# Optimization experiments

Measured on AMD Instinct MI355X. Metric: run time of the kernel, lower is better.

## Reference

```python
import jax, jax.numpy as jnp
import numpy as np
import math

B, L, D, H, DFF = 2, 2048, 1024, 16, 4096

def _mha(xq, xkv, Wq, bq, Wk, bk, Wv, bv, Wo, bo, mask, h):
    # xq: [B,Lq,D], xkv: [B,Lk,D], mask: [B,1,Lq,Lk] bool
    b, lq, d = xq.shape
    dk = d // h
    q = (xq @ Wq + bq).reshape(b, lq, h, dk).transpose(0, 2, 1, 3)        # [B,h,Lq,dk]
    k = (xkv @ Wk + bk).reshape(b, -1, h, dk).transpose(0, 2, 1, 3)       # [B,h,Lk,dk]
    v = (xkv @ Wv + bv).reshape(b, -1, h, dk).transpose(0, 2, 1, 3)       # [B,h,Lk,dk]
    scores = jnp.einsum('bhqd,bhkd->bhqk', q, k) / jnp.sqrt(jnp.float32(dk))
    scores = jnp.where(mask, scores, jnp.float32(-1e9))                   # masked_fill(mask==0, -1e9)
    prob = jax.nn.softmax(scores, axis=-1)
    out = jnp.einsum('bhqk,bhkd->bhqd', prob, v)
    out = out.transpose(0, 2, 1, 3).reshape(b, lq, d)
    return out @ Wo + bo

def setup_inputs() -> dict:
    key = jax.random.key(0)
    ks = jax.random.split(key, 16)
    s = 0.02
    inp = {
        'tgt': jax.random.normal(ks[0], (B, L, D), jnp.float32),
        'encoder_out': jax.random.normal(ks[1], (B, L, D), jnp.float32),
        'tgt_mask': jnp.broadcast_to(jnp.tril(jnp.ones((L, L), bool)), (B, 1, L, L)),
        'src_tgt_mask': jnp.ones((B, 1, L, L), bool),
    }
    names = ['sWq','sWk','sWv','sWo','cWq','cWk','cWv','cWo']
    for i, n in enumerate(names):
        inp[n] = s * jax.random.normal(ks[2 + i], (D, D), jnp.float32)
        inp['sb' + n[2] if n[0] == 's' else 'cb' + n[2]] = jnp.zeros((D,), jnp.float32)
    inp['W1'] = s * jax.random.normal(ks[10], (D, DFF), jnp.float32)
    inp['b1'] = jnp.zeros((DFF,), jnp.float32)
    inp['W2'] = s * jax.random.normal(ks[11], (DFF, D), jnp.float32)
    inp['b2'] = jnp.zeros((D,), jnp.float32)
    return inp

def reference(tgt, encoder_out, tgt_mask, src_tgt_mask,
              sWq, sbq, sWk, sbk, sWv, sbv, sWo, sbo,
              cWq, cbq, cWk, cbk, cWv, cbv, cWo, cbo,
              W1, b1, W2, b2):
    # residual 1: masked self-attention (no norm)
    x = tgt + _mha(tgt, tgt, sWq, sbq, sWk, sbk, sWv, sbv, sWo, sbo, tgt_mask, H)
    # residual 2: cross-attention over encoder_out
    x = x + _mha(x, encoder_out, cWq, cbq, cWk, cbk, cWv, cbv, cWo, cbo, src_tgt_mask, H)
    # residual 3: position-wise FFN with ReLU
    x = x + (jax.nn.relu(x @ W1 + b1) @ W2 + b2)
    return x
```

## Files before the change

kernel.cpp:

```cpp
#include <hip/hip_runtime.h>

typedef unsigned short u16;
typedef unsigned int u32;
typedef __attribute__((ext_vector_type(8))) short short8;
typedef __attribute__((ext_vector_type(8))) __bf16 bf16x8;
typedef __attribute__((ext_vector_type(4))) float f32x4;
typedef __attribute__((ext_vector_type(4))) u16 u16x4;
typedef __attribute__((ext_vector_type(2))) u32 u32x2;

#define GLD16(gp, lp) __builtin_amdgcn_global_load_lds( \
    (const __attribute__((address_space(1))) unsigned int*)(gp), \
    (__attribute__((address_space(3))) unsigned int*)(lp), 16, 0, 0)

#if defined(__has_builtin) && __has_builtin(__builtin_amdgcn_exp2f)
#define EXP2(x) __builtin_amdgcn_exp2f(x)
#else
static __device__ __forceinline__ float exp2_asm(float x){
  float r; asm("v_exp_f32 %0, %1" : "=v"(r) : "v"(x)); return r;
}
#define EXP2(x) exp2_asm(x)
#endif

__device__ __forceinline__ float bf2f(u16 u){
  unsigned x = ((unsigned)u) << 16; float f; __builtin_memcpy(&f, &x, 4); return f;
}
__device__ __forceinline__ u16 f2bf(float f){
  unsigned x; __builtin_memcpy(&x, &f, 4);
  x += 0x7fffu + ((x >> 16) & 1u);
  return (u16)(x >> 16);
}
__device__ __forceinline__ u32 pkhi(float lo, float hi){
  u32 a, b; __builtin_memcpy(&a, &lo, 4); __builtin_memcpy(&b, &hi, 4);
  return __builtin_amdgcn_perm(b, a, 0x07060302u);
}
__device__ __forceinline__ f32x4 mfma_bf16(short8 a, short8 b, f32x4 c){
  return __builtin_amdgcn_mfma_f32_16x16x32_bf16(
      __builtin_bit_cast(bf16x8, a), __builtin_bit_cast(bf16x8, b), c, 0, 0, 0);
}

__global__ __launch_bounds__(256) void k_conv(const float* __restrict__ s, u16* __restrict__ d, int n){
  int i4 = (blockIdx.x * 256 + threadIdx.x) * 4;
  if (i4 < n){
    float4 v = *(const float4*)(s + i4);
    u16x4 o; o.x = f2bf(v.x); o.y = f2bf(v.y); o.z = f2bf(v.z); o.w = f2bf(v.w);
    *(u16x4*)(d + i4) = o;
  }
}

__global__ __launch_bounds__(256) void k_transpose(const float* __restrict__ s, u16* __restrict__ d, int K, int N){
  __shared__ float t[32][33];
  int bx = blockIdx.x * 32, by = blockIdx.y * 32;
  int x = threadIdx.x & 31, y = threadIdx.x >> 5;
  #pragma unroll
  for (int i = 0; i < 4; i++)
    t[y + i*8][x] = s[(size_t)(by + y + i*8) * N + bx + x];
  __syncthreads();
  #pragma unroll
  for (int i = 0; i < 4; i++)
    d[(size_t)(bx + y + i*8) * K + by + x] = f2bf(t[x][y + i*8]);
}

struct TP8 { const float* s[8]; u16* d[8]; };
__global__ __launch_bounds__(256) void k_transpose8(TP8 p){
  __shared__ float t[32][33];
  const float* s = p.s[blockIdx.z];
  u16* d = p.d[blockIdx.z];
  int bx = blockIdx.x * 32, by = blockIdx.y * 32;
  int x = threadIdx.x & 31, y = threadIdx.x >> 5;
  #pragma unroll
  for (int i = 0; i < 4; i++)
    t[y + i*8][x] = s[(size_t)(by + y + i*8) * 1024 + bx + x];
  __syncthreads();
  #pragma unroll
  for (int i = 0; i < 4; i++)
    d[(size_t)(bx + y + i*8) * 1024 + by + x] = f2bf(t[x][y + i*8]);
}

__global__ __launch_bounds__(256) void k_packbias(
    const float* __restrict__ sbq, const float* __restrict__ sbk,
    const float* __restrict__ sbv, const float* __restrict__ cbk,
    const float* __restrict__ cbv, float* __restrict__ pbS,
    float* __restrict__ pbC){
  int i = blockIdx.x * 256 + threadIdx.x;
  if (i < 3072) pbS[i] = (i < 1024) ? sbq[i] : (i < 2048 ? sbk[i-1024] : sbv[i-2048]);
  if (i < 2048) pbC[i] = (i < 1024) ? cbk[i] : cbv[i-1024];
}

template<int EPI, int BM, int BN, int KU>
__global__ __launch_bounds__(256, 2) void k_gemm_bt(
    const u16* __restrict__ A, const u16* __restrict__ BT,
    const float* __restrict__ bias, const float* __restrict__ resid,
    float* __restrict__ outF, u16* __restrict__ outB,
    int M, int N, int K, int vt_start, u16* __restrict__ Vt){
  constexpr int MI = BM / 32, NI = BN / 32;
  __shared__ u16 As[2*KU][BM*32];
  __shared__ u16 Bs[2*KU][BN*32];
  int tid = threadIdx.x, wave = tid >> 6, lane = tid & 63;
  int bm = blockIdx.x * BM, bn = blockIdx.y * BN;
  int wm = (wave & 1) * (BM/2), wn = (wave >> 1) * (BN/2);
  int l15 = lane & 15, quad = lane >> 4;

  f32x4 z = {0.f, 0.f, 0.f, 0.f};
  f32x4 acc[MI][NI];
  #pragma unroll
  for (int a = 0; a < MI; a++)
    #pragma unroll
    for (int b = 0; b < NI; b++) acc[a][b] = z;

  int sr = wave*16 + (lane >> 2);
  int sc = ((lane & 3) ^ ((lane >> 3) & 3)) * 8;
  const u16* Ag = A  + (size_t)(bm + sr) * K + sc;
  const u16* Bg = BT + (size_t)(bn + sr) * K + sc;
  int NKP = (K >> 5) / KU;
  int xsw = (l15 >> 1) & 3;

  #pragma unroll
  for (int u = 0; u < KU; u++){
    #pragma unroll
    for (int i = 0; i < BM/64; i++)
      GLD16(Ag + (size_t)(i*64)*K + u*32, &As[u][(wave*16 + i*64) * 32]);
    #pragma unroll
    for (int i = 0; i < BN/64; i++)
      GLD16(Bg + (size_t)(i*64)*K + u*32, &Bs[u][(wave*16 + i*64) * 32]);
  }

  for (int kt = 0; kt < NKP; kt++){
    __syncthreads();
    int cur = (kt & 1) * KU;
    if (kt + 1 < NKP){
      int nb = cur ^ KU;
      #pragma unroll
      for (int u = 0; u < KU; u++){
        int k0 = ((kt + 1) * KU + u) * 32;
        #pragma unroll
        for (int i = 0; i < BM/64; i++)
          GLD16(Ag + (size_t)(i*64)*K + k0, &As[nb+u][(wave*16 + i*64) * 32]);
        #pragma unroll
        for (int i = 0; i < BN/64; i++)
          GLD16(Bg + (size_t)(i*64)*K + k0, &Bs[nb+u][(wave*16 + i*64) * 32]);
      }
    }
    #pragma unroll
    for (int u = 0; u < KU; u++){
      short8 af[MI], bf[NI];
      #pragma unroll
      for (int mi = 0; mi < MI; mi++)
        af[mi] = *(const short8*)&As[cur+u][(wm + mi*16 + l15)*32 + (quad ^ xsw)*8];
      #pragma unroll
      for (int ni = 0; ni < NI; ni++)
        bf[ni] = *(const short8*)&Bs[cur+u][(wn + ni*16 + l15)*32 + (quad ^ xsw)*8];
      #pragma unroll
      for (int mi = 0; mi < MI; mi++)
        #pragma unroll
        for (int ni = 0; ni < NI; ni++)
          acc[mi][ni] = mfma_bf16(af[mi], bf[ni], acc[mi][ni]);
    }
  }

  #pragma unroll
  for (int mi = 0; mi < MI; mi++){
    #pragma unroll
    for (int ni = 0; ni < NI; ni++){
      int col = bn + wn + ni*16 + l15;
      float bv = bias[col];
      if (EPI == 0 && col >= vt_start){
        int vc = col - vt_start;
        int hh = vc >> 6, dd = vc & 63;
        int row0 = bm + wm + mi*16 + quad*4;
        int bb = row0 >> 11, ll = row0 & 2047;
        u16x4 vv;
        #pragma unroll
        for (int r = 0; r < 4; r++) vv[r] = f2bf(acc[mi][ni][r] + bv);
        *(u16x4*)&Vt[(((size_t)bb*16 + hh)*64 + dd)*2048 + ll] = vv;
      } else {
        #pragma unroll
        for (int r = 0; r < 4; r++){
          int row = bm + wm + mi*16 + quad*4 + r;
          float v = acc[mi][ni][r] + bv;
          if (EPI == 1) v = v > 0.f ? v : 0.f;
          size_t idx = (size_t)row * N + col;
          if (EPI >= 2) v += resid[idx];
          if (EPI == 2 || EPI == 3) outF[idx] = v;
          if (EPI != 3) outB[idx] = f2bf(v);
        }
      }
    }
  }
}

template<bool CAUSAL>
__global__ __launch_bounds__(256, 2) void k_flash(
    const u16* __restrict__ Q, int ldq,
    const u16* __restrict__ Kg, int ldk,
    const u16* __restrict__ Vt,
    u16* __restrict__ O, int ldo){
  __shared__ u16 Ks[2][128*64];
  __shared__ u16 Vs[2][64*128];
  __shared__ u16 Ps[128*64];
  int tid = threadIdx.x, wave = tid >> 6, lane = tid & 63;
  int l15 = lane & 15, quad = lane >> 4;
  int bx = blockIdx.x;
  int qt = CAUSAL ? ((bx & 1) ? (15 - (bx >> 1)) : (bx >> 1)) : bx;
  int bh = blockIdx.y;
  int b = bh >> 4, h = bh & 15;
  size_t bL = (size_t)b * 2048;
  const u16* qp = Q  + (bL + qt*128) * (size_t)ldq + h*64;
  const u16* kp = Kg + bL * (size_t)ldk + h*64;
  const u16* vtp = Vt + (size_t)bh * 64 * 2048;
  int wm = wave * 32;

  const float QSCALE = 0.125f * 1.44269504088896f;
  short8 qf[2][2];
  #pragma unroll
  for (int mi = 0; mi < 2; mi++)
    #pragma unroll
    for (int ks = 0; ks < 2; ks++){
      short8 t = *(const short8*)(qp + (size_t)(wm + mi*16 + l15)*ldq + ks*32 + quad*8);
      #pragma unroll
      for (int j = 0; j < 8; j++)
        t[j] = (short)f2bf(bf2f((u16)t[j]) * QSCALE);
      qf[mi][ks] = t;
    }

  f32x4 z = {0.f, 0.f, 0.f, 0.f};
  f32x4 o[2][4];
  float mrow[2], lrow[2];
  #pragma unroll
  for (int mi = 0; mi < 2; mi++){ mrow[mi] = -3.0e38f; lrow[mi] = 0.f; }
  #pragma unroll
  for (int mi = 0; mi < 2; mi++)
    #pragma unroll
    for (int nd = 0; nd < 4; nd++) o[mi][nd] = z;

  int nkt = CAUSAL ? (qt + 1) : 16;
  int cg = ((lane & 7) ^ ((lane >> 3) & 7)) * 8;
  #pragma unroll
  for (int i = 0; i < 4; i++){
    int r = i*32 + wave*8 + (lane >> 3);
    GLD16(kp + (size_t)r * ldk + cg, &Ks[0][(i*32 + wave*8) * 64]);
  }
  #pragma unroll
  for (int i = 0; i < 4; i++){
    int d0 = i*16 + wave*4;
    int d = d0 + (lane >> 4);
    int j = lane & 15;
    int chunk = (j & 8) | ((j ^ (d & 7)) & 7);
    GLD16(vtp + (size_t)d*2048 + chunk*8, &Vs[0][d0*128]);
  }

  for (int kt = 0; kt < nkt; kt++){
    __syncthreads();
    int cur = kt & 1;
    if (kt + 1 < nkt){
      int nb = cur ^ 1;
      #pragma unroll
      for (int i = 0; i < 4; i++){
        int r = i*32 + wave*8 + (lane >> 3);
        GLD16(kp + (size_t)((kt+1)*128 + r) * ldk + cg, &Ks[nb][(i*32 + wave*8) * 64]);
      }
      #pragma unroll
      for (int i = 0; i < 4; i++){
        int d0 = i*16 + wave*4;
        int d = d0 + (lane >> 4);
        int j = lane & 15;
        int chunk = (j & 8) | ((j ^ (d & 7)) & 7);
        GLD16(vtp + (size_t)d*2048 + (kt+1)*128 + chunk*8, &Vs[nb][d0*128]);
      }
    }

    f32x4 s[2][8];
    #pragma unroll
    for (int mi = 0; mi < 2; mi++)
      #pragma unroll
      for (int nk = 0; nk < 8; nk++) s[mi][nk] = z;
    #pragma unroll
    for (int ks = 0; ks < 2; ks++){
      short8 kf[8];
      #pragma unroll
      for (int nk = 0; nk < 8; nk++){
        int row = nk*16 + l15;
        kf[nk] = *(const short8*)&Ks[cur][row*64 + (((ks*4 + quad) ^ (row & 7)))*8];
      }
      #pragma unroll
      for (int mi = 0; mi < 2; mi++)
        #pragma unroll
        for (int nk = 0; nk < 8; nk++)
          s[mi][nk] = mfma_bf16(kf[nk], qf[mi][ks], s[mi][nk]);
    }

    if (CAUSAL && kt == qt){
      #pragma unroll
      for (int mi = 0; mi < 2; mi++){
        int q = wm + mi*16 + l15;
        #pragma unroll
        for (int nk = 0; nk < 8; nk++)
          #pragma unroll
          for (int r = 0; r < 4; r++){
            int key = nk*16 + quad*4 + r;
            if (key > q) s[mi][nk][r] = -1e30f;
          }
      }
    }

    #pragma unroll
    for (int mi = 0; mi < 2; mi++){
      float mx = s[mi][0][0];
      #pragma unroll
      for (int nk = 0; nk < 8; nk++)
        #pragma unroll
        for (int r = 0; r < 4; r++) mx = fmaxf(mx, s[mi][nk][r]);
      mx = fmaxf(mx, __shfl_xor(mx, 16));
      mx = fmaxf(mx, __shfl_xor(mx, 32));
      if (!__all(mx - mrow[mi] <= 8.f)){
        float mnew = fmaxf(mrow[mi], mx);
        float alpha = EXP2(mrow[mi] - mnew);
        mrow[mi] = mnew;
        lrow[mi] *= alpha;
        #pragma unroll
        for (int r = 0; r < 4; r++){
          float ar = __shfl(alpha, quad*20 + r);
          #pragma unroll
          for (int nd = 0; nd < 4; nd++) o[mi][nd][r] *= ar;
        }
      }
      float ls = 0.f;
      #pragma unroll
      for (int nk = 0; nk < 8; nk++)
        #pragma unroll
        for (int r = 0; r < 4; r++){
          float p = EXP2(s[mi][nk][r] - mrow[mi]);
          s[mi][nk][r] = p;
          ls += p;
        }
      ls += __shfl_xor(ls, 16);
      ls += __shfl_xor(ls, 32);
      lrow[mi] += ls;
    }

    #pragma unroll
    for (int half = 0; half < 2; half++){
      #pragma unroll
      for (int mi = 0; mi < 2; mi++){
        int row = wm + mi*16 + l15;
        #pragma unroll
        for (int nkl = 0; nkl < 4; nkl++){
          int nk = half*4 + nkl;
          u32x2 pw;
          pw.x = pkhi(s[mi][nk][0], s[mi][nk][1]);
          pw.y = pkhi(s[mi][nk][2], s[mi][nk][3]);
          int c = nkl*4 + quad;
          int phys = c ^ (row & 14);
          *(u32x2*)&Ps[row*64 + phys*4] = pw;
        }
      }
      #pragma unroll
      for (int kcl = 0; kcl < 2; kcl++){
        int kc = half*2 + kcl;
        short8 vf[4], pf[2];
        #pragma unroll
        for (int nd = 0; nd < 4; nd++){
          int d = nd*16 + l15;
          int cc = kc*4 + quad;
          int phys = (cc & 8) | ((cc ^ (d & 7)) & 7);
          vf[nd] = *(const short8*)&Vs[cur][d*128 + phys*8];
        }
        #pragma unroll
        for (int mi = 0; mi < 2; mi++){
          int row = wm + mi*16 + l15;
          int pc = kcl*8 + quad*2;
          int pphys = pc ^ (row & 14);
          pf[mi] = *(const short8*)&Ps[row*64 + pphys*4];
        }
        #pragma unroll
        for (int mi = 0; mi < 2; mi++)
          #pragma unroll
          for (int nd = 0; nd < 4; nd++)
            o[mi][nd] = mfma_bf16(pf[mi], vf[nd], o[mi][nd]);
      }
    }
  }

  u16* op = O + (bL + qt*128) * (size_t)ldo + h*64;
  #pragma unroll
  for (int mi = 0; mi < 2; mi++){
    float invl = 1.f / lrow[mi];
    #pragma unroll
    for (int r = 0; r < 4; r++){
      float ir = __shfl(invl, quad*20 + r);
      #pragma unroll
      for (int nd = 0; nd < 4; nd++)
        op[(size_t)(wm + mi*16 + quad*4 + r)*ldo + nd*16 + l15] = f2bf(o[mi][nd][r] * ir);
    }
  }
}

extern "C" void kernel_launch(void* const* d_in, const int* in_sizes, int n_in,
                              void* d_out, int out_size, void* d_ws, size_t ws_size,
                              hipStream_t stream){
  (void)in_sizes; (void)n_in; (void)out_size; (void)ws_size;
  const float* tgt = (const float*)d_in[0];
  const float* enc = (const float*)d_in[1];
  const float* sWq = (const float*)d_in[4];  const float* sbq = (const float*)d_in[5];
  const float* sWk = (const float*)d_in[6];  const float* sbk = (const float*)d_in[7];
  const float* sWv = (const float*)d_in[8];  const float* sbv = (const float*)d_in[9];
  const float* sWo = (const float*)d_in[10]; const float* sbo = (const float*)d_in[11];
  const float* cWq = (const float*)d_in[12]; const float* cbq = (const float*)d_in[13];
  const float* cWk = (const float*)d_in[14]; const float* cbk = (const float*)d_in[15];
  const float* cWv = (const float*)d_in[16]; const float* cbv = (const float*)d_in[17];
  const float* cWo = (const float*)d_in[18]; const float* cbo = (const float*)d_in[19];
  const float* W1  = (const float*)d_in[20]; const float* b1  = (const float*)d_in[21];
  const float* W2  = (const float*)d_in[22]; const float* b2  = (const float*)d_in[23];
  float* out = (float*)d_out;

  const int M = 4096;
  const int NEVER = 1 << 30;
  char* w = (char*)d_ws;
  auto alloc = [&](size_t bytes)->void*{ void* p = w; w += (bytes + 255) & ~(size_t)255; return p; };
  u16* tb    = (u16*)alloc((size_t)M*1024*2);
  u16* eb    = (u16*)alloc((size_t)M*1024*2);
  u16* qkv   = (u16*)alloc((size_t)M*3072*2);
  u16* ao    = (u16*)alloc((size_t)M*1024*2);
  u16* xb    = (u16*)alloc((size_t)M*1024*2);
  float* x1f = (float*)alloc((size_t)M*1024*4);
  u16* hbuf  = (u16*)alloc((size_t)M*4096*2);
  u16* VtS   = (u16*)alloc((size_t)32*64*2048*2);
  u16* VtC   = (u16*)alloc((size_t)32*64*2048*2);
  u16* sQKVT = (u16*)alloc((size_t)3072*1024*2);
  u16* sWoT  = (u16*)alloc((size_t)1024*1024*2);
  u16* cWqT  = (u16*)alloc((size_t)1024*1024*2);
  u16* cKVT  = (u16*)alloc((size_t)2048*1024*2);
  u16* cWoT  = (u16*)alloc((size_t)1024*1024*2);
  u16* W1T   = (u16*)alloc((size_t)4096*1024*2);
  u16* W2T   = (u16*)alloc((size_t)1024*4096*2);
  float* pbS = (float*)alloc(3072*4);
  float* pbC = (float*)alloc(2048*4);
  u16* cq  = tb;
  u16* ckv = qkv;

  k_conv<<<dim3(4096), 256, 0, stream>>>(tgt, tb, M*1024);
  k_conv<<<dim3(4096), 256, 0, stream>>>(enc, eb, M*1024);
  TP8 tp;
  tp.s[0]=sWq; tp.s[1]=sWk; tp.s[2]=sWv; tp.s[3]=sWo;
  tp.s[4]=cWq; tp.s[5]=cWk; tp.s[6]=cWv; tp.s[7]=cWo;
  tp.d[0]=sQKVT; tp.d[1]=sQKVT+1024*1024; tp.d[2]=sQKVT+2048*1024; tp.d[3]=sWoT;
  tp.d[4]=cWqT; tp.d[5]=cKVT; tp.d[6]=cKVT+1024*1024; tp.d[7]=cWoT;
  k_transpose8<<<dim3(32,32,8), 256, 0, stream>>>(tp);
  k_transpose<<<dim3(128,32), 256, 0, stream>>>(W1, W1T, 1024, 4096);
  k_transpose<<<dim3(32,128), 256, 0, stream>>>(W2, W2T, 4096, 1024);
  k_packbias<<<dim3(12), 256, 0, stream>>>(sbq, sbk, sbv, cbk, cbv, pbS, pbC);

  k_gemm_bt<0,128,128,1><<<dim3(32,24), 256, 0, stream>>>(tb, sQKVT, pbS, nullptr, nullptr, qkv, M, 3072, 1024, 2048, VtS);
  k_flash<true><<<dim3(16,32), 256, 0, stream>>>(qkv, 3072, qkv+1024, 3072, VtS, ao, 1024);
  k_gemm_bt<2,64,64,2><<<dim3(64,16), 256, 0, stream>>>(ao, sWoT, sbo, tgt, x1f, xb, M, 1024, 1024, NEVER, nullptr);

  k_gemm_bt<0,64,64,2><<<dim3(64,16), 256, 0, stream>>>(xb, cWqT, cbq, nullptr, nullptr, cq, M, 1024, 1024, NEVER, nullptr);
  k_gemm_bt<0,128,128,1><<<dim3(32,16), 256, 0, stream>>>(eb, cKVT, pbC, nullptr, nullptr, ckv, M, 2048, 1024, 1024, VtC);
  k_flash<false><<<dim3(16,32), 256, 0, stream>>>(cq, 1024, ckv, 2048, VtC, ao, 1024);
  k_gemm_bt<2,64,64,2><<<dim3(64,16), 256, 0, stream>>>(ao, cWoT, cbo, x1f, x1f, xb, M, 1024, 1024, NEVER, nullptr);

  k_gemm_bt<1,128,128,1><<<dim3(32,32), 256, 0, stream>>>(xb, W1T, b1, nullptr, nullptr, hbuf, M, 4096, 1024, NEVER, nullptr);
  k_gemm_bt<3,64,64,2><<<dim3(64,16), 256, 0, stream>>>(hbuf, W2T, b2, x1f, out, nullptr, M, 1024, 4096, NEVER, nullptr);
}
```

Before: 535.1 us.

## Add dedicated 64x64 GEMM kernel with 4-stage async LDS pipeline

Adds a specialized 64x64-tile GEMM that uses a 4-buffer global_load_lds pipeline with explicit vmcnt waits, one barrier per k-step, and an XOR-swizzled LDS layout. It replaces the generic templated GEMM for the four N=1024 projections (self/cross output, cross Q, FFN down). The goal is better latency hiding and occupancy (launch bounds 4) on these small-N GEMMs. It adds a second GEMM code path and relies on hand-tuned waitcnt counts being correct.

After: 545.4 us. Within noise of the previous version (+1.9%).

```diff
diff --git a/kernel.cpp b/kernel.cpp
--- a/kernel.cpp
+++ b/kernel.cpp
@@ -183,6 +183,77 @@
           if (EPI == 2 || EPI == 3) outF[idx] = v;
           if (EPI != 3) outB[idx] = f2bf(v);
         }
+      }
+    }
+  }
+}
+
+template<int EPI>
+__global__ __launch_bounds__(256, 4) void k_gemm64(
+    const u16* __restrict__ A, const u16* __restrict__ BT,
+    const float* __restrict__ bias, const float* __restrict__ resid,
+    float* __restrict__ outF, u16* __restrict__ outB,
+    int M, int N, int K){
+  __shared__ u16 As[4][64*32];
+  __shared__ u16 Bs[4][64*32];
+  int tid = threadIdx.x, wave = tid >> 6, lane = tid & 63;
+  int bm = blockIdx.x * 64, bn = blockIdx.y * 64;
+  int wm = (wave & 1) * 32, wn = (wave >> 1) * 32;
+  int l15 = lane & 15, quad = lane >> 4;
+
+  f32x4 z = {0.f, 0.f, 0.f, 0.f};
+  f32x4 acc[2][2];
+  acc[0][0] = z; acc[0][1] = z; acc[1][0] = z; acc[1][1] = z;
+
+  int sr = wave*16 + (lane >> 2);
+  int sc = ((lane & 3) ^ ((lane >> 3) & 3)) * 8;
+  const u16* Ag = A  + (size_t)(bm + sr) * K + sc;
+  const u16* Bg = BT + (size_t)(bn + sr) * K + sc;
+  int NT = K >> 5;
+  int xsw = (l15 >> 1) & 3;
+
+  #pragma unroll
+  for (int s = 0; s < 3; s++){
+    GLD16(Ag + s*32, &As[s][(wave*16) * 32]);
+    GLD16(Bg + s*32, &Bs[s][(wave*16) * 32]);
+  }
+
+  for (int kt = 0; kt < NT; kt++){
+    if (kt < NT-2)       asm volatile("s_waitcnt vmcnt(4)" ::: "memory");
+    else if (kt == NT-2) asm volatile("s_waitcnt vmcnt(2)" ::: "memory");
+    else                 asm volatile("s_waitcnt vmcnt(0)" ::: "memory");
+    __builtin_amdgcn_s_barrier();
+    if (kt + 3 < NT){
+      int s = (kt + 3) & 3, k0 = (kt + 3) * 32;
+      GLD16(Ag + k0, &As[s][(wave*16) * 32]);
+      GLD16(Bg + k0, &Bs[s][(wave*16) * 32]);
+    }
+    int cur = kt & 3;
+    short8 af[2], bf[2];
+    af[0] = *(const short8*)&As[cur][(wm      + l15)*32 + (quad ^ xsw)*8];
+    af[1] = *(const short8*)&As[cur][(wm + 16 + l15)*32 + (quad ^ xsw)*8];
+    bf[0] = *(const short8*)&Bs[cur][(wn      + l15)*32 + (quad ^ xsw)*8];
+    bf[1] = *(const short8*)&Bs[cur][(wn + 16 + l15)*32 + (quad ^ xsw)*8];
+    acc[0][0] = mfma_bf16(af[0], bf[0], acc[0][0]);
+    acc[0][1] = mfma_bf16(af[0], bf[1], acc[0][1]);
+    acc[1][0] = mfma_bf16(af[1], bf[0], acc[1][0]);
+    acc[1][1] = mfma_bf16(af[1], bf[1], acc[1][1]);
+  }
+
+  #pragma unroll
+  for (int mi = 0; mi < 2; mi++){
+    #pragma unroll
+    for (int ni = 0; ni < 2; ni++){
+      int col = bn + wn + ni*16 + l15;
+      float bv = bias[col];
+      #pragma unroll
+      for (int r = 0; r < 4; r++){
+        int row = bm + wm + mi*16 + quad*4 + r;
+        float v = acc[mi][ni][r] + bv;
+        size_t idx = (size_t)row * N + col;
+        if (EPI >= 2) v += resid[idx];
+        if (EPI == 2 || EPI == 3) outF[idx] = v;
+        if (EPI != 3) outB[idx] = f2bf(v);
       }
     }
   }
@@ -451,13 +522,13 @@
 
   k_gemm_bt<0,128,128,1><<<dim3(32,24), 256, 0, stream>>>(tb, sQKVT, pbS, nullptr, nullptr, qkv, M, 3072, 1024, 2048, VtS);
   k_flash<true><<<dim3(16,32), 256, 0, stream>>>(qkv, 3072, qkv+1024, 3072, VtS, ao, 1024);
-  k_gemm_bt<2,64,64,2><<<dim3(64,16), 256, 0, stream>>>(ao, sWoT, sbo, tgt, x1f, xb, M, 1024, 1024, NEVER, nullptr);
-
-  k_gemm_bt<0,64,64,2><<<dim3(64,16), 256, 0, stream>>>(xb, cWqT, cbq, nullptr, nullptr, cq, M, 1024, 1024, NEVER, nullptr);
+  k_gemm64<2><<<dim3(64,16), 256, 0, stream>>>(ao, sWoT, sbo, tgt, x1f, xb, M, 1024, 1024);
+
+  k_gemm64<0><<<dim3(64,16), 256, 0, stream>>>(xb, cWqT, cbq, nullptr, nullptr, cq, M, 1024, 1024);
   k_gemm_bt<0,128,128,1><<<dim3(32,16), 256, 0, stream>>>(eb, cKVT, pbC, nullptr, nullptr, ckv, M, 2048, 1024, 1024, VtC);
   k_flash<false><<<dim3(16,32), 256, 0, stream>>>(cq, 1024, ckv, 2048, VtC, ao, 1024);
-  k_gemm_bt<2,64,64,2><<<dim3(64,16), 256, 0, stream>>>(ao, cWoT, cbo, x1f, x1f, xb, M, 1024, 1024, NEVER, nullptr);
+  k_gemm64<2><<<dim3(64,16), 256, 0, stream>>>(ao, cWoT, cbo, x1f, x1f, xb, M, 1024, 1024);
 
   k_gemm_bt<1,128,128,1><<<dim3(32,32), 256, 0, stream>>>(xb, W1T, b1, nullptr, nullptr, hbuf, M, 4096, 1024, NEVER, nullptr);
-  k_gemm_bt<3,64,64,2><<<dim3(64,16), 256, 0, stream>>>(hbuf, W2T, b2, x1f, out, nullptr, M, 1024, 4096, NEVER, nullptr);
-}
+  k_gemm64<3><<<dim3(64,16), 256, 0, stream>>>(hbuf, W2T, b2, x1f, out, nullptr, M, 1024, 4096);
+}
```
